# Performance work log

Hardware: AMD Instinct MI355X
Metric: run time of the kernel (lower is better)

The kernel has to match this reference:

```python
import jax, jax.numpy as jnp
import numpy as np

NUM_SEQS = 16
NUM_HEADS = 32
NUM_KV_HEADS = 8
HEAD_SIZE = 128
BLOCK_SIZE = 16
X = 8  # vectorized key-cache packing factor
MAX_CTX = 4096
MAX_BLOCKS = MAX_CTX // BLOCK_SIZE
NUM_BLOCKS = NUM_SEQS * MAX_BLOCKS
SCALE = 0.08838834764831845  # 1/sqrt(128)
NEG_INF = -1e30


def setup_inputs() -> dict:
    key0 = jax.random.key(0)
    ks = jax.random.split(key0, 5)
    query = jax.random.normal(ks[0], (NUM_SEQS, 1, NUM_HEADS * HEAD_SIZE), jnp.float32)
    key = jax.random.normal(ks[1], (NUM_SEQS, 1, NUM_KV_HEADS * HEAD_SIZE), jnp.float32)
    value = jax.random.normal(ks[2], (NUM_SEQS, 1, NUM_KV_HEADS * HEAD_SIZE), jnp.float32)
    key_cache = jax.random.normal(ks[3], (NUM_BLOCKS, NUM_KV_HEADS, HEAD_SIZE // X, BLOCK_SIZE, X), jnp.float32)
    value_cache = jax.random.normal(ks[4], (NUM_BLOCKS, NUM_KV_HEADS, HEAD_SIZE, BLOCK_SIZE), jnp.float32)
    rng = np.random.default_rng(0)
    block_tables = rng.permutation(NUM_BLOCKS).reshape(NUM_SEQS, MAX_BLOCKS).astype(np.int32)
    context_lens = rng.integers(256, MAX_CTX + 1, size=(NUM_SEQS,)).astype(np.int32)
    last = context_lens - 1
    slots = block_tables[np.arange(NUM_SEQS), last // BLOCK_SIZE].astype(np.int64) * BLOCK_SIZE + (last % BLOCK_SIZE)
    slot_mapping = slots.reshape(NUM_SEQS, 1)
    return {
        'query': query, 'key': key, 'value': value,
        'key_cache': key_cache, 'value_cache': value_cache,
        'block_tables': jnp.asarray(block_tables),
        'context_lens': jnp.asarray(context_lens),
        'slot_mapping': jnp.asarray(slot_mapping),
    }


def _paged_attention_decode(query, key, value, key_cache, value_cache, block_tables, context_lens, slot_mapping):
    S, L1, hidden = query.shape  # L1 == 1 (decode)
    nb, kvH, _, bs, x = key_cache.shape
    D = value_cache.shape[2]
    H = hidden // D
    G = H // kvH  # queries per kv head
    maxB = block_tables.shape[1]

    q = query.reshape(S, H, D)
    k_new = key.reshape(S, kvH, D)
    v_new = value.reshape(S, kvH, D)

    # --- reshape_and_cache: write new K/V into paged caches ---
    sm = slot_mapping.reshape(-1)
    blk, off = sm // bs, sm % bs
    key_cache = key_cache.at[blk, :, :, off, :].set(k_new.reshape(S, kvH, D // x, x))
    value_cache = value_cache.at[blk, :, :, off].set(v_new)

    # --- gather paged KV via block tables ---
    # key_cache [nb,kvH,D/x,bs,x] -> [nb,kvH,bs,D]
    kc = key_cache.transpose(0, 1, 3, 2, 4).reshape(nb, kvH, bs, D)
    vc = value_cache.transpose(0, 1, 3, 2)  # [nb,kvH,bs,D]
    keys = kc[block_tables].transpose(0, 1, 3, 2, 4).reshape(S, maxB * bs, kvH, D)
    vals = vc[block_tables].transpose(0, 1, 3, 2, 4).reshape(S, maxB * bs, kvH, D)

    # --- GQA attention with context-length masking ---
    qg = q.reshape(S, kvH, G, D)
    scores = jnp.einsum('skgd,slkd->skgl', qg, keys) * jnp.asarray(SCALE, q.dtype)
    valid = jnp.arange(maxB * bs)[None, :] < context_lens[:, None]  # [S,L]
    scores = jnp.where(valid[:, None, None, :], scores, NEG_INF)
    probs = jax.nn.softmax(scores, axis=-1)
    out = jnp.einsum('skgl,slkd->skgd', probs, vals)
    return out.reshape(S, 1, H * D)


def reference(query, key, value, key_cache, value_cache, block_tables, context_lens, slot_mapping):
    return _paged_attention_decode(query, key, value, key_cache, value_cache,
                                   block_tables, context_lens, slot_mapping)
```

## Files before the change

kernel.cpp:

```cpp
#include <hip/hip_runtime.h>

#define NSEQ   16
#define KVH    8
#define NG     4
#define HD     128
#define BS     16
#define MAXB   256
#define PART   256
#define NPART  16
#define PSTRIDE 520
#define SCALE_F 0.08838834764831845f

__global__ __launch_bounds__(256) void pa_partial_kernel(
    const float* __restrict__ query,
    const float* __restrict__ key,
    const float* __restrict__ value,
    const float* __restrict__ key_cache,
    const float* __restrict__ value_cache,
    const int*   __restrict__ block_tables,
    const int*   __restrict__ context_lens,
    float*       __restrict__ ws)
{
    const int bid = blockIdx.x;
    const int p   = bid & (NPART - 1);
    const int kvh = (bid >> 4) & (KVH - 1);
    const int s   = bid >> 7;

    const int ctx = context_lens[s];
    const int t0  = p * PART;
    if (t0 >= ctx) return;

    __shared__ float q_lds[NG * HD];
    __shared__ float p_lds[NG * PART];
    __shared__ float red[20];

    const int tid = threadIdx.x;

    const float* qsrc = query + (size_t)s * (KVH * NG * HD) + (size_t)kvh * (NG * HD);
    ((float2*)q_lds)[tid] = ((const float2*)qsrc)[tid];
    __syncthreads();

    const int t    = t0 + tid;
    const int bt   = block_tables[s * MAXB + (t >> 4)];
    const int off  = t & 15;
    const bool isnew = (t == ctx - 1);
    const float* kb = isnew ? (key + ((size_t)s * KVH + kvh) * HD)
                            : (key_cache + (size_t)bt * (KVH * HD * BS)
                                         + (size_t)kvh * (HD * BS) + off * 8);
    const int js = isnew ? 8 : 128;

    float sc0 = 0.f, sc1 = 0.f, sc2 = 0.f, sc3 = 0.f;
    const float4* q4 = (const float4*)q_lds;
    #pragma unroll
    for (int j = 0; j < 16; ++j) {
        const float4 ka = *(const float4*)(kb + j * js);
        const float4 kc = *(const float4*)(kb + j * js + 4);
        float4 qa, qb;
        qa = q4[0 * 32 + j * 2]; qb = q4[0 * 32 + j * 2 + 1];
        sc0 += qa.x*ka.x + qa.y*ka.y + qa.z*ka.z + qa.w*ka.w
             + qb.x*kc.x + qb.y*kc.y + qb.z*kc.z + qb.w*kc.w;
        qa = q4[1 * 32 + j * 2]; qb = q4[1 * 32 + j * 2 + 1];
        sc1 += qa.x*ka.x + qa.y*ka.y + qa.z*ka.z + qa.w*ka.w
             + qb.x*kc.x + qb.y*kc.y + qb.z*kc.z + qb.w*kc.w;
        qa = q4[2 * 32 + j * 2]; qb = q4[2 * 32 + j * 2 + 1];
        sc2 += qa.x*ka.x + qa.y*ka.y + qa.z*ka.z + qa.w*ka.w
             + qb.x*kc.x + qb.y*kc.y + qb.z*kc.z + qb.w*kc.w;
        qa = q4[3 * 32 + j * 2]; qb = q4[3 * 32 + j * 2 + 1];
        sc3 += qa.x*ka.x + qa.y*ka.y + qa.z*ka.z + qa.w*ka.w
             + qb.x*kc.x + qb.y*kc.y + qb.z*kc.z + qb.w*kc.w;
    }

    float mval;
    if (t < ctx) {
        sc0 *= SCALE_F; sc1 *= SCALE_F; sc2 *= SCALE_F; sc3 *= SCALE_F;
        mval = fmaxf(fmaxf(sc0, sc1), fmaxf(sc2, sc3));
    } else {
        sc0 = sc1 = sc2 = sc3 = -1e30f;
        mval = -1e30f;
    }

    #pragma unroll
    for (int o = 32; o; o >>= 1) mval = fmaxf(mval, __shfl_xor(mval, o));
    const int wave = tid >> 6;
    if ((tid & 63) == 0) red[wave] = mval;
    __syncthreads();
    const float m = fmaxf(fmaxf(red[0], red[1]), fmaxf(red[2], red[3]));

    const float p0 = __expf(sc0 - m);
    const float p1 = __expf(sc1 - m);
    const float p2 = __expf(sc2 - m);
    const float p3 = __expf(sc3 - m);
    p_lds[0 * PART + tid] = p0;
    p_lds[1 * PART + tid] = p1;
    p_lds[2 * PART + tid] = p2;
    p_lds[3 * PART + tid] = p3;

    float l0 = p0, l1 = p1, l2 = p2, l3 = p3;
    #pragma unroll
    for (int o = 32; o; o >>= 1) {
        l0 += __shfl_xor(l0, o);
        l1 += __shfl_xor(l1, o);
        l2 += __shfl_xor(l2, o);
        l3 += __shfl_xor(l3, o);
    }
    if ((tid & 63) == 0) {
        red[4 + wave * 4 + 0] = l0;
        red[4 + wave * 4 + 1] = l1;
        red[4 + wave * 4 + 2] = l2;
        red[4 + wave * 4 + 3] = l3;
    }
    __syncthreads();

    const int d = tid & 127;
    const int h = tid >> 7;
    float a0 = 0.f, a1 = 0.f, a2 = 0.f, a3 = 0.f;
    const float4* pl4 = (const float4*)p_lds;
    #pragma unroll 2
    for (int b = 0; b < 8; ++b) {
        const int tb   = h * 8 + b;
        const int tg0  = t0 + tb * 16;
        const int btv  = block_tables[s * MAXB + (tg0 >> 4)];
        const float* vb = value_cache + (size_t)btv * (KVH * HD * BS)
                                      + (size_t)kvh * (HD * BS) + d * BS;
        #pragma unroll
        for (int c = 0; c < 4; ++c) {
            const float4 v4  = *(const float4*)(vb + c * 4);
            const float4 pg0 = pl4[0 * 64 + tb * 4 + c];
            const float4 pg1 = pl4[1 * 64 + tb * 4 + c];
            const float4 pg2 = pl4[2 * 64 + tb * 4 + c];
            const float4 pg3 = pl4[3 * 64 + tb * 4 + c];
            a0 += pg0.x*v4.x + pg0.y*v4.y + pg0.z*v4.z + pg0.w*v4.w;
            a1 += pg1.x*v4.x + pg1.y*v4.y + pg1.z*v4.z + pg1.w*v4.w;
            a2 += pg2.x*v4.x + pg2.y*v4.y + pg2.z*v4.z + pg2.w*v4.w;
            a3 += pg3.x*v4.x + pg3.y*v4.y + pg3.z*v4.z + pg3.w*v4.w;
        }
    }

    const int tlnew = ctx - 1 - t0;
    if (tlnew >= h * 128 && tlnew < h * 128 + 128) {
        const int btn = block_tables[s * MAXB + ((ctx - 1) >> 4)];
        const float vold = value_cache[(size_t)btn * (KVH * HD * BS)
                                       + (size_t)kvh * (HD * BS) + d * BS + ((ctx - 1) & 15)];
        const float vnew = value[((size_t)s * KVH + kvh) * HD + d];
        const float dv = vnew - vold;
        a0 += p_lds[0 * PART + tlnew] * dv;
        a1 += p_lds[1 * PART + tlnew] * dv;
        a2 += p_lds[2 * PART + tlnew] * dv;
        a3 += p_lds[3 * PART + tlnew] * dv;
    }

    if (h == 1) {
        q_lds[0 * HD + d] = a0;
        q_lds[1 * HD + d] = a1;
        q_lds[2 * HD + d] = a2;
        q_lds[3 * HD + d] = a3;
    }
    __syncthreads();

    float* rec = ws + (size_t)bid * PSTRIDE;
    if (h == 0) {
        a0 += q_lds[0 * HD + d];
        a1 += q_lds[1 * HD + d];
        a2 += q_lds[2 * HD + d];
        a3 += q_lds[3 * HD + d];
        rec[0 * HD + d] = a0;
        rec[1 * HD + d] = a1;
        rec[2 * HD + d] = a2;
        rec[3 * HD + d] = a3;
    }
    if (tid < 4) {
        rec[512 + tid] = red[4 + tid] + red[8 + tid] + red[12 + tid] + red[16 + tid];
    }
    if (tid == 4) rec[516] = m;
}

__global__ __launch_bounds__(512) void pa_reduce_kernel(
    const float* __restrict__ ws,
    const int*   __restrict__ context_lens,
    float*       __restrict__ out)
{
    const int pair = blockIdx.x;
    const int s    = pair >> 3;
    const int kvh  = pair & 7;
    const int ctx  = context_lens[s];
    const int np   = (ctx + PART - 1) / PART;

    const int tid = threadIdx.x;
    const int g = tid >> 7;
    const int d = tid & 127;

    const float* base = ws + (size_t)pair * NPART * PSTRIDE;

    float M = -1e30f;
    for (int p2 = 0; p2 < np; ++p2) M = fmaxf(M, base[p2 * PSTRIDE + 516]);

    float L = 0.f, acc = 0.f;
    for (int p2 = 0; p2 < np; ++p2) {
        const float* rec = base + p2 * PSTRIDE;
        const float w = __expf(rec[516] - M);
        L   += w * rec[512 + g];
        acc += w * rec[g * HD + d];
    }

    out[(size_t)s * (KVH * NG * HD) + (size_t)(kvh * NG + g) * HD + d] = acc / L;
}

extern "C" void kernel_launch(void* const* d_in, const int* in_sizes, int n_in,
                              void* d_out, int out_size, void* d_ws, size_t ws_size,
                              hipStream_t stream) {
    const float* query       = (const float*)d_in[0];
    const float* key         = (const float*)d_in[1];
    const float* value       = (const float*)d_in[2];
    const float* key_cache   = (const float*)d_in[3];
    const float* value_cache = (const float*)d_in[4];
    const int*   block_tables  = (const int*)d_in[5];
    const int*   context_lens  = (const int*)d_in[6];

    float* out = (float*)d_out;
    float* ws  = (float*)d_ws;

    pa_partial_kernel<<<NSEQ * KVH * NPART, 256, 0, stream>>>(
        query, key, value, key_cache, value_cache, block_tables, context_lens, ws);
    pa_reduce_kernel<<<NSEQ * KVH, 512, 0, stream>>>(ws, context_lens, out);
}
```

Baseline: 90.35 us.

## Read query directly from global, hoist block-table loads, split reduce blocks

Drops the shared-memory staging of the query and its barrier, so every thread reads q directly from global memory through uniform addresses that can become scalar loads. The new-key dot product moves out of the main loop into a separate branch taken by one thread, removing the per-thread stride select. Value-phase block-table indices are loaded up front into registers. The reduce kernel is split into 4x more blocks of 128 threads to spread work across more CUs. The risks are extra global traffic for q and register pressure from the hoisted indices.

```diff
diff --git a/kernel.cpp b/kernel.cpp
--- a/kernel.cpp
+++ b/kernel.cpp
@@ -30,52 +30,57 @@
     const int t0  = p * PART;
     if (t0 >= ctx) return;
 
-    __shared__ float q_lds[NG * HD];
     __shared__ float p_lds[NG * PART];
+    __shared__ float o_lds[NG * HD];
     __shared__ float red[20];
 
     const int tid = threadIdx.x;
-
-    const float* qsrc = query + (size_t)s * (KVH * NG * HD) + (size_t)kvh * (NG * HD);
-    ((float2*)q_lds)[tid] = ((const float2*)qsrc)[tid];
-    __syncthreads();
+    const float* q = query + (size_t)s * (KVH * NG * HD) + (size_t)kvh * (NG * HD);
 
     const int t    = t0 + tid;
     const int bt   = block_tables[s * MAXB + (t >> 4)];
     const int off  = t & 15;
-    const bool isnew = (t == ctx - 1);
-    const float* kb = isnew ? (key + ((size_t)s * KVH + kvh) * HD)
-                            : (key_cache + (size_t)bt * (KVH * HD * BS)
-                                         + (size_t)kvh * (HD * BS) + off * 8);
-    const int js = isnew ? 8 : 128;
-
-    float sc0 = 0.f, sc1 = 0.f, sc2 = 0.f, sc3 = 0.f;
-    const float4* q4 = (const float4*)q_lds;
+    const float* kb = key_cache + (size_t)bt * (KVH * HD * BS)
+                                + (size_t)kvh * (HD * BS) + off * 8;
+
+    float sc[NG] = {0.f, 0.f, 0.f, 0.f};
     #pragma unroll
     for (int j = 0; j < 16; ++j) {
-        const float4 ka = *(const float4*)(kb + j * js);
-        const float4 kc = *(const float4*)(kb + j * js + 4);
-        float4 qa, qb;
-        qa = q4[0 * 32 + j * 2]; qb = q4[0 * 32 + j * 2 + 1];
-        sc0 += qa.x*ka.x + qa.y*ka.y + qa.z*ka.z + qa.w*ka.w
-             + qb.x*kc.x + qb.y*kc.y + qb.z*kc.z + qb.w*kc.w;
-        qa = q4[1 * 32 + j * 2]; qb = q4[1 * 32 + j * 2 + 1];
-        sc1 += qa.x*ka.x + qa.y*ka.y + qa.z*ka.z + qa.w*ka.w
-             + qb.x*kc.x + qb.y*kc.y + qb.z*kc.z + qb.w*kc.w;
-        qa = q4[2 * 32 + j * 2]; qb = q4[2 * 32 + j * 2 + 1];
-        sc2 += qa.x*ka.x + qa.y*ka.y + qa.z*ka.z + qa.w*ka.w
-             + qb.x*kc.x + qb.y*kc.y + qb.z*kc.z + qb.w*kc.w;
-        qa = q4[3 * 32 + j * 2]; qb = q4[3 * 32 + j * 2 + 1];
-        sc3 += qa.x*ka.x + qa.y*ka.y + qa.z*ka.z + qa.w*ka.w
-             + qb.x*kc.x + qb.y*kc.y + qb.z*kc.z + qb.w*kc.w;
+        const float4 ka = *(const float4*)(kb + j * 128);
+        const float4 kc = *(const float4*)(kb + j * 128 + 4);
+        #pragma unroll
+        for (int g = 0; g < NG; ++g) {
+            sc[g] += q[g * HD + j * 8 + 0] * ka.x + q[g * HD + j * 8 + 1] * ka.y
+                   + q[g * HD + j * 8 + 2] * ka.z + q[g * HD + j * 8 + 3] * ka.w
+                   + q[g * HD + j * 8 + 4] * kc.x + q[g * HD + j * 8 + 5] * kc.y
+                   + q[g * HD + j * 8 + 6] * kc.z + q[g * HD + j * 8 + 7] * kc.w;
+        }
+    }
+
+    if (t == ctx - 1) {
+        const float4* kn4 = (const float4*)(key + ((size_t)s * KVH + kvh) * HD);
+        float ns[NG] = {0.f, 0.f, 0.f, 0.f};
+        #pragma unroll
+        for (int c = 0; c < 32; ++c) {
+            const float4 k4 = kn4[c];
+            #pragma unroll
+            for (int g = 0; g < NG; ++g) {
+                ns[g] += q[g * HD + c * 4 + 0] * k4.x + q[g * HD + c * 4 + 1] * k4.y
+                       + q[g * HD + c * 4 + 2] * k4.z + q[g * HD + c * 4 + 3] * k4.w;
+            }
+        }
+        #pragma unroll
+        for (int g = 0; g < NG; ++g) sc[g] = ns[g];
     }
 
     float mval;
     if (t < ctx) {
-        sc0 *= SCALE_F; sc1 *= SCALE_F; sc2 *= SCALE_F; sc3 *= SCALE_F;
-        mval = fmaxf(fmaxf(sc0, sc1), fmaxf(sc2, sc3));
+        #pragma unroll
+        for (int g = 0; g < NG; ++g) sc[g] *= SCALE_F;
+        mval = fmaxf(fmaxf(sc[0], sc[1]), fmaxf(sc[2], sc[3]));
     } else {
-        sc0 = sc1 = sc2 = sc3 = -1e30f;
+        #pragma unroll
+        for (int g = 0; g < NG; ++g) sc[g] = -1e30f;
         mval = -1e30f;
     }
 
@@ -86,10 +91,10 @@
     __syncthreads();
     const float m = fmaxf(fmaxf(red[0], red[1]), fmaxf(red[2], red[3]));
 
-    const float p0 = __expf(sc0 - m);
-    const float p1 = __expf(sc1 - m);
-    const float p2 = __expf(sc2 - m);
-    const float p3 = __expf(sc3 - m);
+    const float p0 = __expf(sc[0] - m);
+    const float p1 = __expf(sc[1] - m);
+    const float p2 = __expf(sc[2] - m);
+    const float p3 = __expf(sc[3] - m);
     p_lds[0 * PART + tid] = p0;
     p_lds[1 * PART + tid] = p1;
     p_lds[2 * PART + tid] = p2;
@@ -113,14 +118,18 @@
 
     const int d = tid & 127;
     const int h = tid >> 7;
+
+    int btv[8];
+    #pragma unroll
+    for (int b = 0; b < 8; ++b)
+        btv[b] = block_tables[s * MAXB + (t0 >> 4) + h * 8 + b];
+
     float a0 = 0.f, a1 = 0.f, a2 = 0.f, a3 = 0.f;
     const float4* pl4 = (const float4*)p_lds;
     #pragma unroll 2
     for (int b = 0; b < 8; ++b) {
-        const int tb   = h * 8 + b;
-        const int tg0  = t0 + tb * 16;
-        const int btv  = block_tables[s * MAXB + (tg0 >> 4)];
-        const float* vb = value_cache + (size_t)btv * (KVH * HD * BS)
+        const int tb = h * 8 + b;
+        const float* vb = value_cache + (size_t)btv[b] * (KVH * HD * BS)
                                       + (size_t)kvh * (HD * BS) + d * BS;
         #pragma unroll
         for (int c = 0; c < 4; ++c) {
@@ -150,19 +159,19 @@
     }
 
     if (h == 1) {
-        q_lds[0 * HD + d] = a0;
-        q_lds[1 * HD + d] = a1;
-        q_lds[2 * HD + d] = a2;
-        q_lds[3 * HD + d] = a3;
+        o_lds[0 * HD + d] = a0;
+        o_lds[1 * HD + d] = a1;
+        o_lds[2 * HD + d] = a2;
+        o_lds[3 * HD + d] = a3;
     }
     __syncthreads();
 
     float* rec = ws + (size_t)bid * PSTRIDE;
     if (h == 0) {
-        a0 += q_lds[0 * HD + d];
-        a1 += q_lds[1 * HD + d];
-        a2 += q_lds[2 * HD + d];
-        a3 += q_lds[3 * HD + d];
+        a0 += o_lds[0 * HD + d];
+        a1 += o_lds[1 * HD + d];
+        a2 += o_lds[2 * HD + d];
+        a3 += o_lds[3 * HD + d];
         rec[0 * HD + d] = a0;
         rec[1 * HD + d] = a1;
         rec[2 * HD + d] = a2;
@@ -174,21 +183,20 @@
     if (tid == 4) rec[516] = m;
 }
 
-__global__ __launch_bounds__(512) void pa_reduce_kernel(
+__global__ __launch_bounds__(128) void pa_reduce_kernel(
     const float* __restrict__ ws,
     const int*   __restrict__ context_lens,
     float*       __restrict__ out)
 {
-    const int pair = blockIdx.x;
+    const int b    = blockIdx.x;
+    const int g    = b & 3;
+    const int pair = b >> 2;
     const int s    = pair >> 3;
     const int kvh  = pair & 7;
     const int ctx  = context_lens[s];
     const int np   = (ctx + PART - 1) / PART;
 
-    const int tid = threadIdx.x;
-    const int g = tid >> 7;
-    const int d = tid & 127;
-
+    const int d = threadIdx.x;
     const float* base = ws + (size_t)pair * NPART * PSTRIDE;
 
     float M = -1e30f;
@@ -221,5 +229,5 @@
 
     pa_partial_kernel<<<NSEQ * KVH * NPART, 256, 0, stream>>>(
         query, key, value, key_cache, value_cache, block_tables, context_lens, ws);
-    pa_reduce_kernel<<<NSEQ * KVH, 512, 0, stream>>>(ws, context_lens, out);
+    pa_reduce_kernel<<<NSEQ * KVH * NG, 128, 0, stream>>>(ws, context_lens, out);
 }
```

After: 90.23 us. About the same (-0.1%).
